# Performance work log

Hardware: AMD Instinct MI355X
Metric: run time of the kernel (lower is better)

Reference implementation:

```python
import jax, jax.numpy as jnp
import numpy as np

HIDDEN = 1024
INTER = 4096
N_EXPERTS = 8
TOP_K = 2


def setup_inputs() -> dict:
    key = jax.random.key(0)
    ks = jax.random.split(key, 5)
    B, S = 2, 1024
    scale_h = 1.0 / np.sqrt(HIDDEN)
    scale_i = 1.0 / np.sqrt(INTER)
    return {
        "hidden_states": jax.random.normal(ks[0], (B, S, HIDDEN), dtype=jnp.float32),
        "router_w": jax.random.normal(ks[1], (N_EXPERTS, HIDDEN), dtype=jnp.float32) * scale_h,
        "gate_w": jax.random.normal(ks[2], (N_EXPERTS, INTER, HIDDEN), dtype=jnp.float32) * scale_h,
        "up_w": jax.random.normal(ks[3], (N_EXPERTS, INTER, HIDDEN), dtype=jnp.float32) * scale_h,
        "down_w": jax.random.normal(ks[4], (N_EXPERTS, HIDDEN, INTER), dtype=jnp.float32) * scale_i,
        "top_k": TOP_K,
    }


def reference(hidden_states, router_w, gate_w, up_w, down_w, top_k):
    B, S, D = hidden_states.shape
    E = router_w.shape[0]
    x = hidden_states.reshape(-1, D)              # [T, D]
    T = x.shape[0]

    router_logits = x @ router_w.T                # [T, E]
    probs = jax.nn.softmax(router_logits.astype(jnp.float32), axis=-1)
    routing_weights, selected = jax.lax.top_k(probs, top_k)   # [T, k]
    routing_weights = routing_weights.astype(x.dtype)

    # Dense combine weights: w[t, e] = routing weight if expert e selected for token t else 0
    combine = jnp.zeros((T, E), x.dtype).at[jnp.arange(T)[:, None], selected].add(routing_weights)

    # SwiGLU expert MLPs, computed for all experts then combined (same math as gather/scatter loop)
    g = jnp.einsum('td,ehd->eth', x, gate_w)      # [E, T, H]
    u = jnp.einsum('td,ehd->eth', x, up_w)        # [E, T, H]
    h = jax.nn.silu(g) * u
    expert_out = jnp.einsum('eth,edh->etd', h, down_w)  # [E, T, D]
    out = jnp.einsum('etd,te->td', expert_out, combine)  # [T, D]

    return out.reshape(B, S, D), router_logits
```

## Files before the change

kernel.cpp:

```cpp
#include <hip/hip_runtime.h>
#include <hip/hip_bf16.h>

#define HIDDEN 1024
#define INTER 4096
#define NEXP 8
#define T_TOK 2048

typedef short bf16x8 __attribute__((ext_vector_type(8)));
typedef float f32x4 __attribute__((ext_vector_type(4)));

#define CHUNK(row, kq) ((unsigned int)((row) * 64u + ((((unsigned int)(kq)) ^ ((((unsigned int)(row)) >> 1) & 3u)) << 4)))

__device__ __forceinline__ unsigned short f2bf(float f) {
    union { float f; unsigned int u; } v; v.f = f;
    return (unsigned short)(v.u >> 16);
}

__device__ __forceinline__ uint4 pack8trunc(float4 a, float4 b) {
    union { float4 f; unsigned short s[8]; } x, y; x.f = a; y.f = b;
    uint4 r;
    r.x = (unsigned int)x.s[1] | ((unsigned int)x.s[3] << 16);
    r.y = (unsigned int)x.s[5] | ((unsigned int)x.s[7] << 16);
    r.z = (unsigned int)y.s[1] | ((unsigned int)y.s[3] << 16);
    r.w = (unsigned int)y.s[5] | ((unsigned int)y.s[7] << 16);
    return r;
}

__device__ __forceinline__ void block_sync() {
    asm volatile("s_waitcnt lgkmcnt(0)" ::: "memory");
    __builtin_amdgcn_s_barrier();
    asm volatile("" ::: "memory");
}

__global__ void router_kernel(const float* __restrict__ x,
                              const float* __restrict__ rw,
                              float* __restrict__ logits_out,
                              int* __restrict__ counts,
                              int* __restrict__ ids,
                              float* __restrict__ wts,
                              int* __restrict__ tsel) {
    int t = blockIdx.x * 4 + (threadIdx.x >> 6);
    int lane = threadIdx.x & 63;
    if (t >= T_TOK) return;
    const float4* xr = (const float4*)(x + (size_t)t * HIDDEN);
    float acc[NEXP];
#pragma unroll
    for (int e = 0; e < NEXP; e++) acc[e] = 0.f;
#pragma unroll
    for (int c = 0; c < 4; c++) {
        float4 xv = xr[lane + c * 64];
#pragma unroll
        for (int e = 0; e < NEXP; e++) {
            float4 wv = ((const float4*)(rw + (size_t)e * HIDDEN))[lane + c * 64];
            acc[e] += xv.x * wv.x + xv.y * wv.y + xv.z * wv.z + xv.w * wv.w;
        }
    }
#pragma unroll
    for (int e = 0; e < NEXP; e++) {
        float v = acc[e];
        for (int off = 32; off >= 1; off >>= 1) v += __shfl_xor(v, off, 64);
        acc[e] = v;
    }
    if (lane == 0) {
        float* lo = logits_out + (size_t)t * NEXP;
        float mx = acc[0];
#pragma unroll
        for (int e = 1; e < NEXP; e++) mx = fmaxf(mx, acc[e]);
        float p[NEXP], s = 0.f;
#pragma unroll
        for (int e = 0; e < NEXP; e++) { p[e] = __expf(acc[e] - mx); s += p[e]; }
        float inv = 1.f / s;
#pragma unroll
        for (int e = 0; e < NEXP; e++) { p[e] *= inv; lo[e] = acc[e]; }
        int i1 = 0;
#pragma unroll
        for (int e = 1; e < NEXP; e++) if (p[e] > p[i1]) i1 = e;
        int i2 = (i1 == 0) ? 1 : 0;
#pragma unroll
        for (int e = 0; e < NEXP; e++) if (e != i1 && e != i2 && p[e] > p[i2]) i2 = e;
        int s1 = atomicAdd(&counts[i1], 1);
        ids[i1 * T_TOK + s1] = t; wts[i1 * T_TOK + s1] = p[i1];
        int s2 = atomicAdd(&counts[i2], 1);
        ids[i2 * T_TOK + s2] = t; wts[i2 * T_TOK + s2] = p[i2];
        tsel[t * 2]     = i1 * T_TOK + s1;
        tsel[t * 2 + 1] = i2 * T_TOK + s2;
    }
}

__global__ void scan_kernel(const int* __restrict__ counts, int* __restrict__ offsets) {
    if (threadIdx.x == 0) {
        int s = 0;
        for (int e = 0; e < NEXP; e++) { offsets[e] = s; s += counts[e]; }
    }
}

__global__ __launch_bounds__(1024) void gemm_gu(
    const float* __restrict__ x, const float* __restrict__ gw, const float* __restrict__ uw,
    const int* __restrict__ counts, const int* __restrict__ offsets,
    const int* __restrict__ ids, unsigned short* __restrict__ h) {
    const int e = blockIdx.z;
    const int cnt = counts[e];
    const int mt = blockIdx.y;
    if (mt * 256 >= cnt) return;
    const int nt = blockIdx.x;
    const int tid = threadIdx.x;
    const int lane = tid & 63, wid = tid >> 6;
    const int wm = wid >> 2, wn = wid & 3;

    __shared__ __align__(16) char lds[65536];

    const int arow = tid >> 2, akq = tid & 3;
    int ali = mt * 256 + arow; if (ali >= cnt) ali = cnt - 1;
    const unsigned int aoff = (unsigned int)(ids[e * T_TOK + ali] * HIDDEN + akq * 8);
    const unsigned int wAo = CHUNK(arow, akq);
    const int bsel = tid >> 9;
    const int bi = tid & 511;
    const int brow = bi >> 2, bkq = bi & 3;
    const float* bsrc = (bsel ? uw : gw) + (size_t)e * INTER * HIDDEN
                        + (size_t)(nt * 128 + brow) * HIDDEN + bkq * 8;
    const unsigned int wBo = 16384u + ((unsigned int)bsel << 13) + CHUNK(brow, bkq);

    f32x4 accg[4][2], accu[4][2];
#pragma unroll
    for (int mf = 0; mf < 4; mf++)
#pragma unroll
        for (int nf = 0; nf < 2; nf++)
#pragma unroll
            for (int v = 0; v < 4; v++) { accg[mf][nf][v] = 0.f; accu[mf][nf][v] = 0.f; }

    float4 aE0, aE1, bE0, bE1, aO0, aO1, bO0, bO1;
    aE0 = *(const float4*)(x + aoff);      aE1 = *(const float4*)(x + aoff + 4);
    bE0 = *(const float4*)(bsrc);          bE1 = *(const float4*)(bsrc + 4);
    aO0 = *(const float4*)(x + aoff + 32); aO1 = *(const float4*)(x + aoff + 36);
    bO0 = *(const float4*)(bsrc + 32);     bO1 = *(const float4*)(bsrc + 36);

#define GU_COMPUTE(BB)                                                                  \
    {                                                                                   \
        const unsigned int kqr = (unsigned int)(lane >> 4);                             \
        const unsigned int rl = (unsigned int)(lane & 15);                              \
        bf16x8 a[4];                                                                    \
        _Pragma("unroll")                                                               \
        for (int mf = 0; mf < 4; mf++)                                                  \
            a[mf] = *(const bf16x8*)(lds + (BB) + CHUNK(wm * 64 + mf * 16 + rl, kqr));  \
        _Pragma("unroll")                                                               \
        for (int nf = 0; nf < 2; nf++) {                                                \
            const unsigned int br = wn * 32 + nf * 16 + rl;                             \
            bf16x8 bg = *(const bf16x8*)(lds + (BB) + 16384 + CHUNK(br, kqr));          \
            bf16x8 bu = *(const bf16x8*)(lds + (BB) + 24576 + CHUNK(br, kqr));          \
            _Pragma("unroll")                                                           \
            for (int mf = 0; mf < 4; mf++) {                                            \
                accg[mf][nf] = __builtin_amdgcn_mfma_f32_16x16x32_bf16(a[mf], bg, accg[mf][nf], 0, 0, 0); \
                accu[mf][nf] = __builtin_amdgcn_mfma_f32_16x16x32_bf16(a[mf], bu, accu[mf][nf], 0, 0, 0); \
            }                                                                           \
        }                                                                               \
    }

    for (int kt = 0; kt < 32; kt += 2) {
        *(uint4*)(lds + wAo) = pack8trunc(aE0, aE1);
        *(uint4*)(lds + wBo) = pack8trunc(bE0, bE1);
        if (kt + 2 < 32) {
            const int ko = (kt + 2) * 32;
            aE0 = *(const float4*)(x + aoff + ko); aE1 = *(const float4*)(x + aoff + ko + 4);
            bE0 = *(const float4*)(bsrc + ko);     bE1 = *(const float4*)(bsrc + ko + 4);
        }
        block_sync();
        GU_COMPUTE(0u)
        *(uint4*)(lds + 32768 + wAo) = pack8trunc(aO0, aO1);
        *(uint4*)(lds + 32768 + wBo) = pack8trunc(bO0, bO1);
        if (kt + 3 < 32) {
            const int ko = (kt + 3) * 32;
            aO0 = *(const float4*)(x + aoff + ko); aO1 = *(const float4*)(x + aoff + ko + 4);
            bO0 = *(const float4*)(bsrc + ko);     bO1 = *(const float4*)(bsrc + ko + 4);
        }
        block_sync();
        GU_COMPUTE(32768u)
    }
#undef GU_COMPUTE

    const int hoff = offsets[e];
#pragma unroll
    for (int mf = 0; mf < 4; mf++)
#pragma unroll
        for (int v = 0; v < 4; v++) {
            int il = wm * 64 + mf * 16 + ((lane >> 4) << 2) + v;
            int i = mt * 256 + il;
            if (i < cnt) {
                size_t rowbase = (size_t)(hoff + i) * INTER + nt * 128 + wn * 32 + (lane & 15);
#pragma unroll
                for (int nf = 0; nf < 2; nf++) {
                    float g = accg[mf][nf][v], u = accu[mf][nf][v];
                    float sg = g / (1.f + __expf(-g));
                    h[rowbase + nf * 16] = f2bf(sg * u);
                }
            }
        }
}

__global__ __launch_bounds__(512) void gemm_down(
    const unsigned short* __restrict__ h, const float* __restrict__ dw,
    const int* __restrict__ counts, const int* __restrict__ offsets,
    const float* __restrict__ wts, float* __restrict__ y) {
    const int ez = blockIdx.z;
    const int e = ez >> 1, ksp = ez & 1;
    const int cnt = counts[e];
    const int mt = blockIdx.y;
    if (mt * 128 >= cnt) return;
    const int nt = blockIdx.x;
    const int tid = threadIdx.x;
    const int lane = tid & 63, wid = tid >> 6;
    const int wm = wid >> 2, wn = wid & 3;

    __shared__ __align__(16) char lds[32768];

    const int hoff = offsets[e];
    const float* dbase = dw + (size_t)e * HIDDEN * INTER;

    const int row = tid >> 2, kq = tid & 3;
    int li = mt * 128 + row; if (li >= cnt) li = cnt - 1;
    const unsigned int aoff = (unsigned int)((hoff + li) * INTER + ksp * 2048 + kq * 8);
    const unsigned int wAo = CHUNK(row, kq);
    const unsigned int boff = (unsigned int)((nt * 128 + row) * INTER + ksp * 2048 + kq * 8);
    const unsigned int wBo = 8192u + CHUNK(row, kq);

    f32x4 acc[4][2];
#pragma unroll
    for (int mf = 0; mf < 4; mf++)
#pragma unroll
        for (int nf = 0; nf < 2; nf++)
#pragma unroll
            for (int v = 0; v < 4; v++) acc[mf][nf][v] = 0.f;

    int4 avE, avO; float4 bE0, bE1, bO0, bO1;
    avE = *(const int4*)(h + aoff);
    bE0 = *(const float4*)(dbase + boff);      bE1 = *(const float4*)(dbase + boff + 4);
    avO = *(const int4*)(h + aoff + 32);
    bO0 = *(const float4*)(dbase + boff + 32); bO1 = *(const float4*)(dbase + boff + 36);

#define DN_COMPUTE(BB)                                                                  \
    {                                                                                   \
        const unsigned int kqr = (unsigned int)(lane >> 4);                             \
        const unsigned int rl = (unsigned int)(lane & 15);                              \
        bf16x8 a[4];                                                                    \
        _Pragma("unroll")                                                               \
        for (int mf = 0; mf < 4; mf++)                                                  \
            a[mf] = *(const bf16x8*)(lds + (BB) + CHUNK(wm * 64 + mf * 16 + rl, kqr));  \
        _Pragma("unroll")                                                               \
        for (int nf = 0; nf < 2; nf++) {                                                \
            bf16x8 b = *(const bf16x8*)(lds + (BB) + 8192 + CHUNK(wn * 32 + nf * 16 + rl, kqr)); \
            _Pragma("unroll")                                                           \
            for (int mf = 0; mf < 4; mf++)                                              \
                acc[mf][nf] = __builtin_amdgcn_mfma_f32_16x16x32_bf16(a[mf], b, acc[mf][nf], 0, 0, 0); \
        }                                                                               \
    }

    for (int kt = 0; kt < 64; kt += 2) {
        *(int4*)(lds + wAo) = avE;
        *(uint4*)(lds + wBo) = pack8trunc(bE0, bE1);
        if (kt + 2 < 64) {
            const int ko = (kt + 2) * 32;
            avE = *(const int4*)(h + aoff + ko);
            bE0 = *(const float4*)(dbase + boff + ko); bE1 = *(const float4*)(dbase + boff + ko + 4);
        }
        block_sync();
        DN_COMPUTE(0u)
        *(int4*)(lds + 16384 + wAo) = avO;
        *(uint4*)(lds + 16384 + wBo) = pack8trunc(bO0, bO1);
        if (kt + 3 < 64) {
            const int ko = (kt + 3) * 32;
            avO = *(const int4*)(h + aoff + ko);
            bO0 = *(const float4*)(dbase + boff + ko); bO1 = *(const float4*)(dbase + boff + ko + 4);
        }
        block_sync();
        DN_COMPUTE(16384u)
    }
#undef DN_COMPUTE

#pragma unroll
    for (int mf = 0; mf < 4; mf++)
#pragma unroll
        for (int v = 0; v < 4; v++) {
            int il = wm * 64 + mf * 16 + ((lane >> 4) << 2) + v;
            int i = mt * 128 + il;
            if (i < cnt) {
                float w = wts[e * T_TOK + i];
                float* yrow = y + ((size_t)ksp * 4096 + hoff + i) * HIDDEN
                                + nt * 128 + wn * 32 + (lane & 15);
#pragma unroll
                for (int nf = 0; nf < 2; nf++)
                    yrow[nf * 16] = w * acc[mf][nf][v];
            }
        }
}

__global__ __launch_bounds__(256) void combine_kernel(
    const float* __restrict__ y, const int* __restrict__ offsets,
    const int* __restrict__ tsel, float* __restrict__ out) {
    const int t = blockIdx.x;
    const int d = threadIdx.x * 4;
    int p0 = tsel[t * 2], p1 = tsel[t * 2 + 1];
    size_t g0 = (size_t)(offsets[p0 >> 11] + (p0 & (T_TOK - 1)));
    size_t g1 = (size_t)(offsets[p1 >> 11] + (p1 & (T_TOK - 1)));
    float4 a0 = *(const float4*)(y + g0 * HIDDEN + d);
    float4 a1 = *(const float4*)(y + (4096 + g0) * HIDDEN + d);
    float4 b0 = *(const float4*)(y + g1 * HIDDEN + d);
    float4 b1 = *(const float4*)(y + (4096 + g1) * HIDDEN + d);
    float4 o;
    o.x = (a0.x + a1.x) + (b0.x + b1.x);
    o.y = (a0.y + a1.y) + (b0.y + b1.y);
    o.z = (a0.z + a1.z) + (b0.z + b1.z);
    o.w = (a0.w + a1.w) + (b0.w + b1.w);
    *(float4*)(out + (size_t)t * HIDDEN + d) = o;
}

extern "C" void kernel_launch(void* const* d_in, const int* in_sizes, int n_in,
                              void* d_out, int out_size, void* d_ws, size_t ws_size,
                              hipStream_t stream) {
    const float* x  = (const float*)d_in[0];
    const float* rw = (const float*)d_in[1];
    const float* gw = (const float*)d_in[2];
    const float* uw = (const float*)d_in[3];
    const float* dw = (const float*)d_in[4];
    float* out = (float*)d_out;
    float* logits = out + (size_t)T_TOK * HIDDEN;

    char* ws = (char*)d_ws;
    int*   counts  = (int*)ws;
    int*   offsets = (int*)(ws + 32);
    int*   tsel    = (int*)(ws + 1024);
    int*   ids     = (int*)(ws + 20480);
    float* wts     = (float*)(ws + 90112);
    unsigned short* h = (unsigned short*)(ws + 262144);
    float* y       = (float*)(ws + 262144 + 33554432);

    hipMemsetAsync(counts, 0, 8 * sizeof(int), stream);

    router_kernel<<<T_TOK / 4, 256, 0, stream>>>(x, rw, logits, counts, ids, wts, tsel);
    scan_kernel<<<1, 64, 0, stream>>>(counts, offsets);
    gemm_gu<<<dim3(INTER / 128, 8, NEXP), 1024, 0, stream>>>(x, gw, uw, counts, offsets, ids, h);
    gemm_down<<<dim3(HIDDEN / 128, 16, NEXP * 2), 512, 0, stream>>>(h, dw, counts, offsets, wts, y);
    combine_kernel<<<T_TOK, 256, 0, stream>>>(y, offsets, tsel, out);
}
```

Baseline: 358.0 us.

## Shrink gate/up GEMM tile to 128 rows with 512 threads and single-stage double buffer

```diff
diff --git a/kernel.cpp b/kernel.cpp
--- a/kernel.cpp
+++ b/kernel.cpp
@@ -94,31 +94,29 @@
     }
 }
 
-__global__ __launch_bounds__(1024) void gemm_gu(
+__global__ __launch_bounds__(512, 4) void gemm_gu(
     const float* __restrict__ x, const float* __restrict__ gw, const float* __restrict__ uw,
     const int* __restrict__ counts, const int* __restrict__ offsets,
     const int* __restrict__ ids, unsigned short* __restrict__ h) {
     const int e = blockIdx.z;
     const int cnt = counts[e];
     const int mt = blockIdx.y;
-    if (mt * 256 >= cnt) return;
+    if (mt * 128 >= cnt) return;
     const int nt = blockIdx.x;
     const int tid = threadIdx.x;
     const int lane = tid & 63, wid = tid >> 6;
     const int wm = wid >> 2, wn = wid & 3;
 
-    __shared__ __align__(16) char lds[65536];
-
-    const int arow = tid >> 2, akq = tid & 3;
-    int ali = mt * 256 + arow; if (ali >= cnt) ali = cnt - 1;
-    const unsigned int aoff = (unsigned int)(ids[e * T_TOK + ali] * HIDDEN + akq * 8);
-    const unsigned int wAo = CHUNK(arow, akq);
-    const int bsel = tid >> 9;
-    const int bi = tid & 511;
-    const int brow = bi >> 2, bkq = bi & 3;
-    const float* bsrc = (bsel ? uw : gw) + (size_t)e * INTER * HIDDEN
-                        + (size_t)(nt * 128 + brow) * HIDDEN + bkq * 8;
-    const unsigned int wBo = 16384u + ((unsigned int)bsel << 13) + CHUNK(brow, bkq);
+    __shared__ __align__(16) char lds[49152];
+
+    const float* gbase = gw + (size_t)e * INTER * HIDDEN;
+    const float* ubase = uw + (size_t)e * INTER * HIDDEN;
+
+    const int row = tid >> 2, kq = tid & 3;
+    int ali = mt * 128 + row; if (ali >= cnt) ali = cnt - 1;
+    const unsigned int aoff = (unsigned int)(ids[e * T_TOK + ali] * HIDDEN + kq * 8);
+    const unsigned int boff = (unsigned int)((nt * 128 + row) * HIDDEN + kq * 8);
+    const unsigned int wC = CHUNK(row, kq);
 
     f32x4 accg[4][2], accu[4][2];
 #pragma unroll
@@ -128,54 +126,41 @@
 #pragma unroll
             for (int v = 0; v < 4; v++) { accg[mf][nf][v] = 0.f; accu[mf][nf][v] = 0.f; }
 
-    float4 aE0, aE1, bE0, bE1, aO0, aO1, bO0, bO1;
-    aE0 = *(const float4*)(x + aoff);      aE1 = *(const float4*)(x + aoff + 4);
-    bE0 = *(const float4*)(bsrc);          bE1 = *(const float4*)(bsrc + 4);
-    aO0 = *(const float4*)(x + aoff + 32); aO1 = *(const float4*)(x + aoff + 36);
-    bO0 = *(const float4*)(bsrc + 32);     bO1 = *(const float4*)(bsrc + 36);
-
-#define GU_COMPUTE(BB)                                                                  \
-    {                                                                                   \
-        const unsigned int kqr = (unsigned int)(lane >> 4);                             \
-        const unsigned int rl = (unsigned int)(lane & 15);                              \
-        bf16x8 a[4];                                                                    \
-        _Pragma("unroll")                                                               \
-        for (int mf = 0; mf < 4; mf++)                                                  \
-            a[mf] = *(const bf16x8*)(lds + (BB) + CHUNK(wm * 64 + mf * 16 + rl, kqr));  \
-        _Pragma("unroll")                                                               \
-        for (int nf = 0; nf < 2; nf++) {                                                \
-            const unsigned int br = wn * 32 + nf * 16 + rl;                             \
-            bf16x8 bg = *(const bf16x8*)(lds + (BB) + 16384 + CHUNK(br, kqr));          \
-            bf16x8 bu = *(const bf16x8*)(lds + (BB) + 24576 + CHUNK(br, kqr));          \
-            _Pragma("unroll")                                                           \
-            for (int mf = 0; mf < 4; mf++) {                                            \
-                accg[mf][nf] = __builtin_amdgcn_mfma_f32_16x16x32_bf16(a[mf], bg, accg[mf][nf], 0, 0, 0); \
-                accu[mf][nf] = __builtin_amdgcn_mfma_f32_16x16x32_bf16(a[mf], bu, accu[mf][nf], 0, 0, 0); \
-            }                                                                           \
-        }                                                                               \
-    }
-
-    for (int kt = 0; kt < 32; kt += 2) {
-        *(uint4*)(lds + wAo) = pack8trunc(aE0, aE1);
-        *(uint4*)(lds + wBo) = pack8trunc(bE0, bE1);
-        if (kt + 2 < 32) {
-            const int ko = (kt + 2) * 32;
-            aE0 = *(const float4*)(x + aoff + ko); aE1 = *(const float4*)(x + aoff + ko + 4);
-            bE0 = *(const float4*)(bsrc + ko);     bE1 = *(const float4*)(bsrc + ko + 4);
+    float4 a0, a1, g0, g1, u0, u1;
+    a0 = *(const float4*)(x + aoff);      a1 = *(const float4*)(x + aoff + 4);
+    g0 = *(const float4*)(gbase + boff);  g1 = *(const float4*)(gbase + boff + 4);
+    u0 = *(const float4*)(ubase + boff);  u1 = *(const float4*)(ubase + boff + 4);
+
+    for (int kt = 0; kt < 32; kt++) {
+        const unsigned int bb = (unsigned int)(kt & 1) * 24576u;
+        *(uint4*)(lds + bb + wC) = pack8trunc(a0, a1);
+        *(uint4*)(lds + bb + 8192 + wC) = pack8trunc(g0, g1);
+        *(uint4*)(lds + bb + 16384 + wC) = pack8trunc(u0, u1);
+        if (kt < 31) {
+            const int ko = (kt + 1) * 32;
+            a0 = *(const float4*)(x + aoff + ko);      a1 = *(const float4*)(x + aoff + ko + 4);
+            g0 = *(const float4*)(gbase + boff + ko);  g1 = *(const float4*)(gbase + boff + ko + 4);
+            u0 = *(const float4*)(ubase + boff + ko);  u1 = *(const float4*)(ubase + boff + ko + 4);
         }
         block_sync();
-        GU_COMPUTE(0u)
-        *(uint4*)(lds + 32768 + wAo) = pack8trunc(aO0, aO1);
-        *(uint4*)(lds + 32768 + wBo) = pack8trunc(bO0, bO1);
-        if (kt + 3 < 32) {
-            const int ko = (kt + 3) * 32;
-            aO0 = *(const float4*)(x + aoff + ko); aO1 = *(const float4*)(x + aoff + ko + 4);
-            bO0 = *(const float4*)(bsrc + ko);     bO1 = *(const float4*)(bsrc + ko + 4);
-        }
-        block_sync();
-        GU_COMPUTE(32768u)
-    }
-#undef GU_COMPUTE
+        const unsigned int kqr = (unsigned int)(lane >> 4);
+        const unsigned int rl = (unsigned int)(lane & 15);
+        bf16x8 a[4];
+#pragma unroll
+        for (int mf = 0; mf < 4; mf++)
+            a[mf] = *(const bf16x8*)(lds + bb + CHUNK(wm * 64 + mf * 16 + rl, kqr));
+#pragma unroll
+        for (int nf = 0; nf < 2; nf++) {
+            const unsigned int br = wn * 32 + nf * 16 + rl;
+            bf16x8 bg = *(const bf16x8*)(lds + bb + 8192 + CHUNK(br, kqr));
+            bf16x8 bu = *(const bf16x8*)(lds + bb + 16384 + CHUNK(br, kqr));
+#pragma unroll
+            for (int mf = 0; mf < 4; mf++) {
+                accg[mf][nf] = __builtin_amdgcn_mfma_f32_16x16x32_bf16(a[mf], bg, accg[mf][nf], 0, 0, 0);
+                accu[mf][nf] = __builtin_amdgcn_mfma_f32_16x16x32_bf16(a[mf], bu, accu[mf][nf], 0, 0, 0);
+            }
+        }
+    }
 
     const int hoff = offsets[e];
 #pragma unroll
@@ -183,7 +168,7 @@
 #pragma unroll
         for (int v = 0; v < 4; v++) {
             int il = wm * 64 + mf * 16 + ((lane >> 4) << 2) + v;
-            int i = mt * 256 + il;
+            int i = mt * 128 + il;
             if (i < cnt) {
                 size_t rowbase = (size_t)(hoff + i) * INTER + nt * 128 + wn * 32 + (lane & 15);
 #pragma unroll
@@ -336,7 +321,7 @@
 
     router_kernel<<<T_TOK / 4, 256, 0, stream>>>(x, rw, logits, counts, ids, wts, tsel);
     scan_kernel<<<1, 64, 0, stream>>>(counts, offsets);
-    gemm_gu<<<dim3(INTER / 128, 8, NEXP), 1024, 0, stream>>>(x, gw, uw, counts, offsets, ids, h);
+    gemm_gu<<<dim3(INTER / 128, 16, NEXP), 512, 0, stream>>>(x, gw, uw, counts, offsets, ids, h);
     gemm_down<<<dim3(HIDDEN / 128, 16, NEXP * 2), 512, 0, stream>>>(h, dw, counts, offsets, wts, y);
     combine_kernel<<<T_TOK, 256, 0, stream>>>(y, offsets, tsel, out);
 }
```

New measurement: 315.3 us. 1.14x faster.
